# Performance work log

Measured on AMD Instinct MI355X. Metric: run time of the kernel, lower is better.

The kernel has to match this reference:

```python
import jax, jax.numpy as jnp
import numpy as np
from jax import lax

DIM = 1024      # model dim
DS = 16         # d_state
DC = 4          # d_conv
EXP = 2
DI = DIM * EXP  # d_inner = 2048
B, L = 2, 1024


def setup_inputs() -> dict:
    key = jax.random.key(0)
    ks = jax.random.split(key, 10)
    s = lambda k, shape, sc: jax.random.normal(k, shape, jnp.float32) * sc
    return {
        "x": s(ks[0], (B, L, DIM), 1.0),
        "norm_w": jnp.ones((DIM,), jnp.float32),
        "norm_b": jnp.zeros((DIM,), jnp.float32),
        "in_proj_w": s(ks[1], (2 * DI, DIM), DIM ** -0.5),
        "conv_w": s(ks[2], (DI, 1, DC), DC ** -0.5),   # depthwise: (out=DI, in/groups=1, K)
        "conv_b": jnp.zeros((DI,), jnp.float32),
        "x_proj_w": s(ks[3], (2 * DS + 1, DI), DI ** -0.5),
        "dt_w": s(ks[4], (DI, 1), 1.0),
        "dt_b": jax.random.uniform(ks[5], (DI,), jnp.float32, -0.001, 0.001),
        "A_log": s(ks[6], (DI, DS), 1.0),              # self.A (randn); A = -exp(A_log)
        "D_skip": jnp.ones((DI,), jnp.float32),
        "out_proj_w": s(ks[7], (DIM, DI), DI ** -0.5),
    }


def _ssm(x, x_proj_w, dt_w, dt_b, A_log, D_skip):
    # x: (B, L, DI)
    xp = jnp.einsum('bli,pi->blp', x, x_proj_w)            # (B, L, 2*DS+1)
    delta = jax.nn.softplus(xp[..., :1] * dt_w[:, 0] + dt_b)  # (B, L, DI)
    Bp = xp[..., 1:DS + 1]                                  # (B, L, DS)
    Cp = xp[..., DS + 1:]                                   # (B, L, DS)
    A = -jnp.exp(A_log)                                     # (DI, DS)
    dA = jnp.exp(delta[..., None] * A)                      # (B, L, DI, DS)
    dB = delta[..., None] * Bp[:, :, None, :] * x[..., None]  # (B, L, DI, DS)

    def step(h, inp):
        dA_t, dB_t, C_t = inp                               # (B,DI,DS),(B,DI,DS),(B,DS)
        h = dA_t * h + dB_t
        return h, jnp.einsum('bdn,bn->bd', h, C_t)

    h0 = jnp.zeros((x.shape[0], DI, DS), x.dtype)
    _, ys = lax.scan(step, h0, (jnp.swapaxes(dA, 0, 1),
                                jnp.swapaxes(dB, 0, 1),
                                jnp.swapaxes(Cp, 0, 1)))
    y = jnp.swapaxes(ys, 0, 1)                              # (B, L, DI)
    return y + x * D_skip


def reference(x, norm_w, norm_b, in_proj_w, conv_w, conv_b,
              x_proj_w, dt_w, dt_b, A_log, D_skip, out_proj_w):
    # LayerNorm
    mu = x.mean(-1, keepdims=True)
    var = ((x - mu) ** 2).mean(-1, keepdims=True)
    xn = (x - mu) * lax.rsqrt(var + 1e-5) * norm_w + norm_b
    # input projection and gate split
    xz = jnp.einsum('bld,pd->blp', xn, in_proj_w)           # (B, L, 2*DI)
    xi, z = xz[..., :DI], xz[..., DI:]
    # causal depthwise conv (torch pads K-1 both sides then slices [:L] == left-pad K-1)
    xc = lax.conv_general_dilated(jnp.swapaxes(xi, 1, 2), conv_w, (1,),
                                  [(DC - 1, 0)], feature_group_count=DI,
                                  dimension_numbers=('NCH', 'OIH', 'NCH'))
    xc = jnp.swapaxes(xc + conv_b[None, :, None], 1, 2)     # (B, L, DI)
    xc = jax.nn.silu(xc)
    y = _ssm(xc, x_proj_w, dt_w, dt_b, A_log, D_skip)
    y = y * jax.nn.silu(z)
    return x + jnp.einsum('bli,di->bld', y, out_proj_w)
```

## Files before the change

kernel.cpp:

```cpp
#include <hip/hip_runtime.h>
#include <stdint.h>

#define BATCH 2
#define SEQ   1024
#define DIM_  1024
#define DS_   16
#define DI_   2048
#define NTOK  (BATCH*SEQ)
#define NSEG  32
#define LSEG  (SEQ/NSEG)

typedef unsigned short u16;
using s16x8 = __attribute__((ext_vector_type(8))) short;
using f32x4 = __attribute__((ext_vector_type(4))) float;
using u16x4 = __attribute__((ext_vector_type(4))) unsigned short;
using u16x8 = __attribute__((ext_vector_type(8))) unsigned short;

__device__ __forceinline__ float bf2f(u16 u) {
  union { unsigned int i; float f; } c; c.i = ((unsigned int)u) << 16; return c.f;
}
__device__ __forceinline__ u16 f2bf(float f) {
  union { float f; unsigned int i; } c; c.f = f;
  unsigned int r = c.i + 0x7fffu + ((c.i >> 16) & 1u);
  return (u16)(r >> 16);
}
__device__ __forceinline__ float softplus_f(float x) {
  return (x > 15.f) ? x : __logf(1.f + __expf(x));
}
__device__ __forceinline__ u16x4 f4_to_bf(float4 v) {
  u16x4 r; r[0] = f2bf(v.x); r[1] = f2bf(v.y); r[2] = f2bf(v.z); r[3] = f2bf(v.w);
  return r;
}

#define N4_INW  (2 * DI_ * DIM_ / 4)
#define N4_OUTW (DIM_ * DI_ / 4)
#define CVT_BLOCKS ((N4_INW + N4_OUTW + 32768) / 256)
__global__ __launch_bounds__(256) void cvt_ln_kernel(const float* __restrict__ in_w,
    const float* __restrict__ out_w, const float* __restrict__ xproj_w,
    const float* __restrict__ x, const float* __restrict__ nw,
    const float* __restrict__ nb, u16* __restrict__ in_w_bf,
    u16* __restrict__ out_w_bf, u16* __restrict__ xpw_bf, u16* __restrict__ xn) {
  int tid = threadIdx.x;
  if (blockIdx.x < CVT_BLOCKS) {
    int i = blockIdx.x * 256 + tid;
    if (i < N4_INW) {
      ((u16x4*)in_w_bf)[i] = f4_to_bf(((const float4*)in_w)[i]);
    } else if (i < N4_INW + N4_OUTW) {
      int j = i - N4_INW;
      ((u16x4*)out_w_bf)[j] = f4_to_bf(((const float4*)out_w)[j]);
    } else {
      int j = i - (N4_INW + N4_OUTW);
      if (j >= 32768) return;
      int p = (j * 4) >> 11;
      u16x4 r;
      if (p < 33) r = f4_to_bf(((const float4*)xproj_w)[j]);
      else { r[0] = 0; r[1] = 0; r[2] = 0; r[3] = 0; }
      ((u16x4*)xpw_bf)[j] = r;
    }
    return;
  }
  int t = blockIdx.x - CVT_BLOCKS;
  const float* row = x + (size_t)t * DIM_;
  float4 v = ((const float4*)row)[tid];
  float f[4] = {v.x, v.y, v.z, v.w};
  float s = 0.f, sq = 0.f;
#pragma unroll
  for (int j = 0; j < 4; j++) { s += f[j]; sq += f[j] * f[j]; }
#pragma unroll
  for (int m = 1; m < 64; m <<= 1) { s += __shfl_xor(s, m); sq += __shfl_xor(sq, m); }
  __shared__ float rs_[4], rq_[4];
  int wv = tid >> 6;
  if ((tid & 63) == 0) { rs_[wv] = s; rq_[wv] = sq; }
  __syncthreads();
  s = rs_[0] + rs_[1] + rs_[2] + rs_[3];
  sq = rq_[0] + rq_[1] + rq_[2] + rq_[3];
  float mu = s * (1.0f / DIM_);
  float var = sq * (1.0f / DIM_) - mu * mu;
  float rstd = rsqrtf(var + 1e-5f);
  float4 wn = ((const float4*)nw)[tid];
  float4 bn = ((const float4*)nb)[tid];
  u16x4 o;
  o[0] = f2bf((f[0] - mu) * rstd * wn.x + bn.x);
  o[1] = f2bf((f[1] - mu) * rstd * wn.y + bn.y);
  o[2] = f2bf((f[2] - mu) * rstd * wn.z + bn.z);
  o[3] = f2bf((f[3] - mu) * rstd * wn.w + bn.w);
  *(u16x4*)(xn + (size_t)t * DIM_ + tid * 4) = o;
}

template<int TBM, int TBN, int BK, typename OUT, int EPI, int KSPLIT = 1, int SWZ = 0>
__global__ __launch_bounds__(256) void gemm_bt(const u16* __restrict__ A,
    const u16* __restrict__ Wt, OUT* __restrict__ C, const float* __restrict__ X,
    int M, int N, int K) {
  constexpr int LDT = BK + 8;
  constexpr int TPR = BK / 8;
  constexpr int RPP = 256 / TPR;
  constexpr int ALn = TBM / RPP;
  constexpr int BLn = TBN / RPP;
  constexpr int KK = BK / 32;
  constexpr int WM = TBM / 2, WN = TBN / 2;
  constexpr int MI = WM / 16, NJ = WN / 16;
  __shared__ __align__(16) u16 sA[TBM * LDT];
  __shared__ __align__(16) u16 sB[TBN * LDT];
  const int tid = threadIdx.x;
  const int lane = tid & 63, wv = tid >> 6;
  const int wm = (wv >> 1) * WM, wn = (wv & 1) * WN;
  const int bxl = SWZ ? ((blockIdx.x & 7) * (gridDim.x >> 3) + (blockIdx.x >> 3))
                      : blockIdx.x;
  const int bm0 = blockIdx.y * TBM, bn0 = bxl * TBN;
  const int q = lane >> 4, r16 = lane & 15;
  const int srow = tid / TPR, scol = (tid % TPR) * 8;
  const int kc = K / KSPLIT;
  const int k0 = (KSPLIT > 1) ? blockIdx.z * kc : 0;
  const int kend = k0 + kc;

  f32x4 acc[MI][NJ];
#pragma unroll
  for (int i = 0; i < MI; i++)
#pragma unroll
    for (int j = 0; j < NJ; j++)
#pragma unroll
      for (int r = 0; r < 4; r++) acc[i][j][r] = 0.f;

  const u16* Ag = A + (size_t)bm0 * K + scol + k0;
  const u16* Wg = Wt + (size_t)bn0 * K + scol + k0;
  s16x8 ra[ALn], rb[BLn];
#pragma unroll
  for (int i = 0; i < ALn; i++) ra[i] = *(const s16x8*)(Ag + (size_t)(srow + i * RPP) * K);
#pragma unroll
  for (int i = 0; i < BLn; i++) rb[i] = *(const s16x8*)(Wg + (size_t)(srow + i * RPP) * K);

  for (int kt = k0; kt < kend; kt += BK) {
    __syncthreads();
#pragma unroll
    for (int i = 0; i < ALn; i++) *(s16x8*)&sA[(srow + i * RPP) * LDT + scol] = ra[i];
#pragma unroll
    for (int i = 0; i < BLn; i++) *(s16x8*)&sB[(srow + i * RPP) * LDT + scol] = rb[i];
    __syncthreads();
    int kn = kt + BK - k0;
    if (kn < kc) {
#pragma unroll
      for (int i = 0; i < ALn; i++) ra[i] = *(const s16x8*)(Ag + (size_t)(srow + i * RPP) * K + kn);
#pragma unroll
      for (int i = 0; i < BLn; i++) rb[i] = *(const s16x8*)(Wg + (size_t)(srow + i * RPP) * K + kn);
    }
#pragma unroll
    for (int kk = 0; kk < KK; kk++) {
      s16x8 fa[MI], fb[NJ];
#pragma unroll
      for (int i = 0; i < MI; i++)
        fa[i] = *(const s16x8*)&sA[(wm + i * 16 + r16) * LDT + kk * 32 + q * 8];
#pragma unroll
      for (int j = 0; j < NJ; j++)
        fb[j] = *(const s16x8*)&sB[(wn + j * 16 + r16) * LDT + kk * 32 + q * 8];
#pragma unroll
      for (int i = 0; i < MI; i++)
#pragma unroll
        for (int j = 0; j < NJ; j++)
          acc[i][j] = __builtin_amdgcn_mfma_f32_16x16x32_bf16(fa[i], fb[j], acc[i][j], 0, 0, 0);
    }
  }
  OUT* Cz = C + ((KSPLIT > 1) ? (size_t)blockIdx.z * M * N : 0);
#pragma unroll
  for (int i = 0; i < MI; i++)
#pragma unroll
    for (int j = 0; j < NJ; j++) {
      int row0 = bm0 + wm + i * 16 + q * 4;
      int col = bn0 + wn + j * 16 + r16;
#pragma unroll
      for (int r = 0; r < 4; r++) {
        size_t off = (size_t)(row0 + r) * N + col;
        float v = acc[i][j][r];
        if constexpr (EPI == 1) v += X[off];
        if constexpr (sizeof(OUT) == 2) Cz[off] = f2bf(v);
        else                            Cz[off] = v;
      }
    }
}

__global__ __launch_bounds__(256) void conv_silu_kernel(const u16* __restrict__ xz,
    const float* __restrict__ cw, const float* __restrict__ cb, u16* __restrict__ xc) {
  int t = blockIdx.x;
  int l = t & (SEQ - 1);
  int c0 = threadIdx.x * 8;
  float acc[8], wk[8][4];
#pragma unroll
  for (int j = 0; j < 8; j++) {
    float4 wv = ((const float4*)cw)[c0 + j];
    wk[j][0] = wv.x; wk[j][1] = wv.y; wk[j][2] = wv.z; wk[j][3] = wv.w;
    acc[j] = cb[c0 + j];
  }
#pragma unroll
  for (int k = 0; k < 4; k++) {
    int lk = l - 3 + k;
    if (lk >= 0) {
      u16x8 v = *(const u16x8*)(xz + (size_t)(t - 3 + k) * (2 * DI_) + c0);
#pragma unroll
      for (int j = 0; j < 8; j++) acc[j] = fmaf(bf2f(v[j]), wk[j][k], acc[j]);
    }
  }
  u16x8 o;
#pragma unroll
  for (int j = 0; j < 8; j++) {
    float a = acc[j];
    o[j] = f2bf(a / (1.0f + __expf(-a)));
  }
  *(u16x8*)(xc + (size_t)t * DI_ + c0) = o;
}

__global__ __launch_bounds__(256) void xp_finish_kernel(const float* __restrict__ part,
    const float* __restrict__ dtw, const float* __restrict__ dtb,
    u16* __restrict__ xz, float* __restrict__ bc) {
  int t = blockIdx.x;
  int tid = threadIdx.x;
  __shared__ float xps[64];
  if (tid < 64) {
    float s = 0.f;
#pragma unroll
    for (int k = 0; k < 8; k++)
      s += part[(size_t)k * NTOK * 64 + (size_t)t * 64 + tid];
    xps[tid] = s;
  }
  __syncthreads();
  if (tid < 32) bc[(size_t)t * 32 + tid] = xps[1 + tid];
  float dr = xps[0];
  int c0 = tid * 8;
  float wv[8], bv[8];
  *(float4*)wv = ((const float4*)(dtw + c0))[0];
  *(float4*)(wv + 4) = ((const float4*)(dtw + c0))[1];
  *(float4*)bv = ((const float4*)(dtb + c0))[0];
  *(float4*)(bv + 4) = ((const float4*)(dtb + c0))[1];
  u16x8 o;
#pragma unroll
  for (int j = 0; j < 8; j++) o[j] = f2bf(softplus_f(dr * wv[j] + bv[j]));
  *(u16x8*)(xz + (size_t)t * (2 * DI_) + c0) = o;
}

#define SRT 72
#define SBC 36

__global__ __launch_bounds__(256) void scan_pass1(const float* __restrict__ bc,
    const u16* __restrict__ dlt, const u16* __restrict__ xc,
    const float* __restrict__ A_log, float* __restrict__ P, float* __restrict__ Q) {
  __shared__ __align__(16) u16 sD[LSEG * SRT];
  __shared__ __align__(16) u16 sX[LSEG * SRT];
  __shared__ __align__(16) float sB[LSEG * SBC];
  int tid = threadIdx.x;
  int lane = tid & 63, wv = tid >> 6;
  int nl = (lane & 3) * 4;
  int dl = wv * 16 + (lane >> 2);
  int d0 = blockIdx.x * 64;
  int s = blockIdx.y, b = blockIdx.z;
  int t0 = b * SEQ + s * LSEG;
  {
    int tr = tid >> 3, c = (tid & 7) * 8;
    *(u16x8*)&sD[tr * SRT + c] = *(const u16x8*)(dlt + (size_t)(t0 + tr) * (2 * DI_) + d0 + c);
    *(u16x8*)&sX[tr * SRT + c] = *(const u16x8*)(xc  + (size_t)(t0 + tr) * DI_ + d0 + c);
    int tb = tid & 31, cb = (tid >> 5) * 4;
    *(f32x4*)&sB[tb * SBC + cb] = *(const f32x4*)(bc + (size_t)(t0 + tb) * 32 + cb);
  }
  int d = d0 + dl;
  float4 Ain = *(const float4*)(A_log + d * DS_ + nl);
  f32x4 Av;
  Av[0] = -__expf(Ain.x); Av[1] = -__expf(Ain.y);
  Av[2] = -__expf(Ain.z); Av[3] = -__expf(Ain.w);
  f32x4 Pv, h;
#pragma unroll
  for (int i = 0; i < 4; i++) { Pv[i] = 1.f; h[i] = 0.f; }
  __syncthreads();
#pragma unroll 8
  for (int j = 0; j < LSEG; j++) {
    float delta = bf2f(sD[j * SRT + dl]);
    float xcv   = bf2f(sX[j * SRT + dl]);
    f32x4 B4 = *(const f32x4*)&sB[j * SBC + nl];
    float du = delta * xcv;
#pragma unroll
    for (int i = 0; i < 4; i++) {
      float a = __expf(delta * Av[i]);
      Pv[i] *= a;
      h[i] = fmaf(a, h[i], du * B4[i]);
    }
  }
  size_t idx = ((size_t)((b * NSEG + s) * DI_ + d)) * 16 + nl;
  *(f32x4*)(P + idx) = Pv;
  *(f32x4*)(Q + idx) = h;
}

__global__ __launch_bounds__(256) void scan_pass2(const float* __restrict__ bc,
    const u16* __restrict__ dlt, const u16* __restrict__ xc,
    const float* __restrict__ A_log, const float* __restrict__ Dskip,
    const float* __restrict__ P, const float* __restrict__ Q,
    u16* __restrict__ yb) {
  __shared__ __align__(16) u16 sD[LSEG * SRT];
  __shared__ __align__(16) u16 sX[LSEG * SRT];
  __shared__ __align__(16) u16 sZ[LSEG * SRT];
  __shared__ __align__(16) float sB[LSEG * SBC];
  int tid = threadIdx.x;
  int lane = tid & 63, wv = tid >> 6;
  int nl = (lane & 3) * 4;
  int dl = wv * 16 + (lane >> 2);
  int d0 = blockIdx.x * 64;
  int s = blockIdx.y, b = blockIdx.z;
  int t0 = b * SEQ + s * LSEG;
  {
    int tr = tid >> 3, c = (tid & 7) * 8;
    *(u16x8*)&sD[tr * SRT + c] = *(const u16x8*)(dlt + (size_t)(t0 + tr) * (2 * DI_) + d0 + c);
    *(u16x8*)&sZ[tr * SRT + c] = *(const u16x8*)(dlt + (size_t)(t0 + tr) * (2 * DI_) + DI_ + d0 + c);
    *(u16x8*)&sX[tr * SRT + c] = *(const u16x8*)(xc  + (size_t)(t0 + tr) * DI_ + d0 + c);
    int tb = tid & 31, cb = (tid >> 5) * 4;
    *(f32x4*)&sB[tb * SBC + cb] = *(const f32x4*)(bc + (size_t)(t0 + tb) * 32 + cb);
  }
  int d = d0 + dl;
  float4 Ain = *(const float4*)(A_log + d * DS_ + nl);
  f32x4 Av;
  Av[0] = -__expf(Ain.x); Av[1] = -__expf(Ain.y);
  Av[2] = -__expf(Ain.z); Av[3] = -__expf(Ain.w);
  float Dv = Dskip[d];
  f32x4 h;
#pragma unroll
  for (int i = 0; i < 4; i++) h[i] = 0.f;
  for (int s2 = 0; s2 < s; s2++) {
    size_t ix = ((size_t)((b * NSEG + s2) * DI_ + d)) * 16 + nl;
    f32x4 Pv = *(const f32x4*)(P + ix);
    f32x4 Qv = *(const f32x4*)(Q + ix);
#pragma unroll
    for (int i = 0; i < 4; i++) h[i] = fmaf(Pv[i], h[i], Qv[i]);
  }
  __syncthreads();
#pragma unroll 8
  for (int j = 0; j < LSEG; j++) {
    float delta = bf2f(sD[j * SRT + dl]);
    float xcv   = bf2f(sX[j * SRT + dl]);
    f32x4 B4 = *(const f32x4*)&sB[j * SBC + nl];
    f32x4 C4 = *(const f32x4*)&sB[j * SBC + 16 + nl];
    float du = delta * xcv;
#pragma unroll
    for (int i = 0; i < 4; i++) {
      float a = __expf(delta * Av[i]);
      h[i] = fmaf(a, h[i], du * B4[i]);
    }
    float p = h[0] * C4[0];
    p = fmaf(h[1], C4[1], p);
    p = fmaf(h[2], C4[2], p);
    p = fmaf(h[3], C4[3], p);
    p += __shfl_xor(p, 1);
    p += __shfl_xor(p, 2);
    if ((lane & 3) == 0) {
      float z = bf2f(sZ[j * SRT + dl]);
      float sz = z / (1.0f + __expf(-z));
      yb[(size_t)(t0 + j) * DI_ + d] = f2bf((p + xcv * Dv) * sz);
    }
  }
}

extern "C" void kernel_launch(void* const* d_in, const int* in_sizes, int n_in,
                              void* d_out, int out_size, void* d_ws, size_t ws_size,
                              hipStream_t stream) {
  const float* x      = (const float*)d_in[0];
  const float* norm_w = (const float*)d_in[1];
  const float* norm_b = (const float*)d_in[2];
  const float* in_w   = (const float*)d_in[3];
  const float* conv_w = (const float*)d_in[4];
  const float* conv_b = (const float*)d_in[5];
  const float* xproj_w= (const float*)d_in[6];
  const float* dt_w   = (const float*)d_in[7];
  const float* dt_b   = (const float*)d_in[8];
  const float* A_log  = (const float*)d_in[9];
  const float* D_skip = (const float*)d_in[10];
  const float* out_w  = (const float*)d_in[11];
  float* out = (float*)d_out;

  char* ws = (char*)d_ws;
  size_t off = 0;
  auto alloc = [&](size_t bytes) { void* p = ws + off; off += (bytes + 255) & ~255ULL; return p; };
  u16* in_w_bf  = (u16*)alloc((size_t)2 * DI_ * DIM_ * 2);
  u16* out_w_bf = (u16*)alloc((size_t)DIM_ * DI_ * 2);
  u16* xpw_bf   = (u16*)alloc((size_t)64 * DI_ * 2);
  u16* xn       = (u16*)alloc((size_t)NTOK * DIM_ * 2);
  u16* xz       = (u16*)alloc((size_t)NTOK * 2 * DI_ * 2);
  u16* xc       = (u16*)alloc((size_t)NTOK * DI_ * 2);
  float* bc     = (float*)alloc((size_t)NTOK * 32 * 4);
  float* xp_part= (float*)alloc((size_t)8 * NTOK * 64 * 4);
  float* P      = (float*)alloc((size_t)BATCH * NSEG * DI_ * 16 * 4);
  float* Q      = (float*)alloc((size_t)BATCH * NSEG * DI_ * 16 * 4);
  u16* yb       = (u16*)alloc((size_t)NTOK * DI_ * 2);

  cvt_ln_kernel<<<CVT_BLOCKS + NTOK, 256, 0, stream>>>(in_w, out_w, xproj_w, x,
                                                       norm_w, norm_b, in_w_bf,
                                                       out_w_bf, xpw_bf, xn);
  gemm_bt<128, 128, 64, u16, 0, 1, 1><<<dim3((2 * DI_) / 128, NTOK / 128), 256, 0, stream>>>(
      xn, in_w_bf, xz, nullptr, NTOK, 2 * DI_, DIM_);
  conv_silu_kernel<<<NTOK, 256, 0, stream>>>(xz, conv_w, conv_b, xc);
  gemm_bt<64, 64, 32, float, 0, 8><<<dim3(1, NTOK / 64, 8), 256, 0, stream>>>(
      xc, xpw_bf, xp_part, nullptr, NTOK, 64, DI_);
  xp_finish_kernel<<<NTOK, 256, 0, stream>>>(xp_part, dt_w, dt_b, xz, bc);
  scan_pass1<<<dim3(DI_ / 64, NSEG, BATCH), 256, 0, stream>>>(bc, xz, xc, A_log, P, Q);
  scan_pass2<<<dim3(DI_ / 64, NSEG, BATCH), 256, 0, stream>>>(bc, xz, xc, A_log, D_skip,
                                                              P, Q, yb);
  gemm_bt<64, 64, 64, float, 1, 1, 1><<<dim3(DIM_ / 64, NTOK / 64), 256, 0, stream>>>(
      yb, out_w_bf, out, x, NTOK, DIM_, DI_);
}
```

Before: 225.3 us.

## Fuse causal depthwise conv and SiLU into the x_proj split-K GEMM

Replaces the standalone conv+SiLU kernel and the x_proj GEMM with one kernel that computes the conv+SiLU for each A-tile on the fly while loading it. The result goes straight into shared memory for MFMA and is also written out as xc for the later scan kernels. This removes one launch and one global read of xc. In exchange, each GEMM block does conv work including redundant weight loads per channel, and only 256 blocks do all the conv work, which may limit parallelism.

```diff
diff --git a/kernel.cpp b/kernel.cpp
--- a/kernel.cpp
+++ b/kernel.cpp
@@ -177,34 +177,103 @@
     }
 }
 
-__global__ __launch_bounds__(256) void conv_silu_kernel(const u16* __restrict__ xz,
-    const float* __restrict__ cw, const float* __restrict__ cb, u16* __restrict__ xc) {
-  int t = blockIdx.x;
-  int l = t & (SEQ - 1);
-  int c0 = threadIdx.x * 8;
-  float acc[8], wk[8][4];
-#pragma unroll
-  for (int j = 0; j < 8; j++) {
-    float4 wv = ((const float4*)cw)[c0 + j];
-    wk[j][0] = wv.x; wk[j][1] = wv.y; wk[j][2] = wv.z; wk[j][3] = wv.w;
-    acc[j] = cb[c0 + j];
-  }
-#pragma unroll
-  for (int k = 0; k < 4; k++) {
-    int lk = l - 3 + k;
-    if (lk >= 0) {
-      u16x8 v = *(const u16x8*)(xz + (size_t)(t - 3 + k) * (2 * DI_) + c0);
-#pragma unroll
-      for (int j = 0; j < 8; j++) acc[j] = fmaf(bf2f(v[j]), wk[j][k], acc[j]);
-    }
-  }
-  u16x8 o;
-#pragma unroll
-  for (int j = 0; j < 8; j++) {
-    float a = acc[j];
-    o[j] = f2bf(a / (1.0f + __expf(-a)));
-  }
-  *(u16x8*)(xc + (size_t)t * DI_ + c0) = o;
+__global__ __launch_bounds__(256) void convxp_gemm(const u16* __restrict__ xz,
+    const float* __restrict__ cw, const float* __restrict__ cb,
+    const u16* __restrict__ Wt, float* __restrict__ C, u16* __restrict__ xc) {
+  constexpr int BK = 32, LDT = BK + 8;
+  constexpr int WM = 32, WN = 32, MI = 2, NJ = 2;
+  constexpr int K = DI_, Nn = 64;
+  __shared__ __align__(16) u16 sA[64 * LDT];
+  __shared__ __align__(16) u16 sB[64 * LDT];
+  const int tid = threadIdx.x;
+  const int lane = tid & 63, wv = tid >> 6;
+  const int wm = (wv >> 1) * WM, wn = (wv & 1) * WN;
+  const int bm0 = blockIdx.y * 64;
+  const int q = lane >> 4, r16 = lane & 15;
+  const int srow = tid >> 2, scol = (tid & 3) * 8;
+  const int kc = K / 8;
+  const int k0 = blockIdx.z * kc;
+
+  f32x4 acc[MI][NJ];
+#pragma unroll
+  for (int i = 0; i < MI; i++)
+#pragma unroll
+    for (int j = 0; j < NJ; j++)
+#pragma unroll
+      for (int r = 0; r < 4; r++) acc[i][j][r] = 0.f;
+
+  const int tm = bm0 + srow;
+  const int l = tm & (SEQ - 1);
+  const u16* Wg = Wt + (size_t)srow * K + scol + k0;
+
+  auto conv8 = [&](int kt) -> s16x8 {
+    int ch = k0 + kt + scol;
+    float a[8];
+    float4 cb0 = *(const float4*)(cb + ch);
+    float4 cb1 = *(const float4*)(cb + ch + 4);
+    a[0] = cb0.x; a[1] = cb0.y; a[2] = cb0.z; a[3] = cb0.w;
+    a[4] = cb1.x; a[5] = cb1.y; a[6] = cb1.z; a[7] = cb1.w;
+#pragma unroll
+    for (int k = 0; k < 4; k++) {
+      if (l - 3 + k >= 0) {
+        u16x8 v = *(const u16x8*)(xz + (size_t)(tm - 3 + k) * (2 * DI_) + ch);
+#pragma unroll
+        for (int j = 0; j < 8; j++) {
+          float4 wj = ((const float4*)cw)[ch + j];
+          float wk = (k == 0) ? wj.x : (k == 1) ? wj.y : (k == 2) ? wj.z : wj.w;
+          a[j] = fmaf(bf2f(v[j]), wk, a[j]);
+        }
+      }
+    }
+    u16x8 o;
+#pragma unroll
+    for (int j = 0; j < 8; j++) {
+      float s = a[j] / (1.0f + __expf(-a[j]));
+      o[j] = f2bf(s);
+    }
+    *(u16x8*)(xc + (size_t)tm * DI_ + ch) = o;
+    return *(s16x8*)&o;
+  };
+
+  s16x8 ra = conv8(0);
+  s16x8 rb = *(const s16x8*)Wg;
+
+  for (int kt = 0; kt < kc; kt += BK) {
+    __syncthreads();
+    *(s16x8*)&sA[srow * LDT + scol] = ra;
+    *(s16x8*)&sB[srow * LDT + scol] = rb;
+    __syncthreads();
+    int kn = kt + BK;
+    if (kn < kc) {
+      ra = conv8(kn);
+      rb = *(const s16x8*)(Wg + kn);
+    }
+    {
+      s16x8 fa[MI], fb[NJ];
+#pragma unroll
+      for (int i = 0; i < MI; i++)
+        fa[i] = *(const s16x8*)&sA[(wm + i * 16 + r16) * LDT + q * 8];
+#pragma unroll
+      for (int j = 0; j < NJ; j++)
+        fb[j] = *(const s16x8*)&sB[(wn + j * 16 + r16) * LDT + q * 8];
+#pragma unroll
+      for (int i = 0; i < MI; i++)
+#pragma unroll
+        for (int j = 0; j < NJ; j++)
+          acc[i][j] = __builtin_amdgcn_mfma_f32_16x16x32_bf16(fa[i], fb[j], acc[i][j], 0, 0, 0);
+    }
+  }
+  float* Cz = C + (size_t)blockIdx.z * NTOK * Nn;
+#pragma unroll
+  for (int i = 0; i < MI; i++)
+#pragma unroll
+    for (int j = 0; j < NJ; j++) {
+      int row0 = bm0 + wm + i * 16 + q * 4;
+      int col = wn + j * 16 + r16;
+#pragma unroll
+      for (int r = 0; r < 4; r++)
+        Cz[(size_t)(row0 + r) * Nn + col] = acc[i][j][r];
+    }
 }
 
 __global__ __launch_bounds__(256) void xp_finish_kernel(const float* __restrict__ part,
@@ -389,9 +458,8 @@
                                                        out_w_bf, xpw_bf, xn);
   gemm_bt<128, 128, 64, u16, 0, 1, 1><<<dim3((2 * DI_) / 128, NTOK / 128), 256, 0, stream>>>(
       xn, in_w_bf, xz, nullptr, NTOK, 2 * DI_, DIM_);
-  conv_silu_kernel<<<NTOK, 256, 0, stream>>>(xz, conv_w, conv_b, xc);
-  gemm_bt<64, 64, 32, float, 0, 8><<<dim3(1, NTOK / 64, 8), 256, 0, stream>>>(
-      xc, xpw_bf, xp_part, nullptr, NTOK, 64, DI_);
+  convxp_gemm<<<dim3(1, NTOK / 64, 8), 256, 0, stream>>>(
+      xz, conv_w, conv_b, xpw_bf, xp_part, xc);
   xp_finish_kernel<<<NTOK, 256, 0, stream>>>(xp_part, dt_w, dt_b, xz, bc);
   scan_pass1<<<dim3(DI_ / 64, NSEG, BATCH), 256, 0, stream>>>(bc, xz, xc, A_log, P, Q);
   scan_pass2<<<dim3(DI_ / 64, NSEG, BATCH), 256, 0, stream>>>(bc, xz, xc, A_log, D_skip,
```

After: 217.9 us. 3.3% less time.
